# Optimization experiments

Measured on AMD Instinct MI355X. Metric: run time of the kernel, lower is better.

Reference implementation:

```python
import jax, jax.numpy as jnp
import numpy as np

B, S, H, NH = 2, 2048, 1024, 16
HD = H // NH  # 64
BASE = 10000.0


def _rope_tables(seq_len, head_dim):
    inv_freq = 1.0 / (BASE ** (jnp.arange(0, head_dim, 2, dtype=jnp.float32) / head_dim))
    t = jnp.arange(seq_len, dtype=jnp.float32)
    freqs = jnp.outer(t, inv_freq)            # [S, HD/2]
    emb = jnp.concatenate([freqs, freqs], -1)  # [S, HD]
    return jnp.cos(emb), jnp.sin(emb)


def _rotate_half(x):
    x1, x2 = jnp.split(x, 2, axis=-1)
    return jnp.concatenate([-x2, x1], axis=-1)


def setup_inputs() -> dict:
    key = jax.random.key(0)
    ks = jax.random.split(key, 5)
    sc = 1.0 / np.sqrt(H)
    return {
        "hidden_states": jax.random.normal(ks[0], (B, S, H), jnp.float32),
        "Wq": jax.random.normal(ks[1], (H, H), jnp.float32) * sc,
        "Wk": jax.random.normal(ks[2], (H, H), jnp.float32) * sc,
        "Wv": jax.random.normal(ks[3], (H, H), jnp.float32) * sc,
        "Wo": jax.random.normal(ks[4], (H, H), jnp.float32) * sc,
    }


def reference(hidden_states, Wq, Wk, Wv, Wo):
    b, s, h = hidden_states.shape
    # nn.Linear: y = x @ W.T
    q = hidden_states @ Wq.T
    k = hidden_states @ Wk.T
    v = hidden_states @ Wv.T
    # [B, NH, S, HD]
    q = q.reshape(b, s, NH, HD).transpose(0, 2, 1, 3)
    k = k.reshape(b, s, NH, HD).transpose(0, 2, 1, 3)
    v = v.reshape(b, s, NH, HD).transpose(0, 2, 1, 3)
    cos, sin = _rope_tables(s, HD)  # [S, HD], broadcast over B, NH
    q = q * cos + _rotate_half(q) * sin
    k = k * cos + _rotate_half(k) * sin
    scores = jnp.einsum('bhqd,bhkd->bhqk', q, k) / jnp.sqrt(jnp.float32(HD))
    probs = jax.nn.softmax(scores, axis=-1)
    ctx = jnp.einsum('bhqk,bhkd->bhqd', probs, v)
    ctx = ctx.transpose(0, 2, 1, 3).reshape(b, s, h)
    return ctx @ Wo.T
```

## Files before the change

### kernel.cpp

```cpp
#include <hip/hip_runtime.h>
#include <hip/hip_bf16.h>
#include <math.h>

typedef __hip_bfloat16 bf16;
typedef float f32x4 __attribute__((ext_vector_type(4)));
typedef float f32x16 __attribute__((ext_vector_type(16)));
typedef short s16x8 __attribute__((ext_vector_type(8)));

#define NB 2
#define SEQ 2048
#define HID 1024
#define NHEAD 16
#define HD 64
#define BH (NB * NHEAD)
#define MROWS (NB * SEQ)
#define QSCL 0.18033688011111793f

static __device__ __forceinline__ f32x4 mfma16(s16x8 a, s16x8 b, f32x4 c) {
  return __builtin_amdgcn_mfma_f32_16x16x32_bf16(a, b, c, 0, 0, 0);
}
static __device__ __forceinline__ f32x16 mfma32(s16x8 a, s16x8 b, f32x16 c) {
  return __builtin_amdgcn_mfma_f32_32x32x16_bf16(a, b, c, 0, 0, 0);
}

static __device__ __forceinline__ void gload_lds16(const bf16* g, bf16* l) {
  __builtin_amdgcn_global_load_lds((const __attribute__((address_space(1))) void*)g,
                                   (__attribute__((address_space(3))) void*)l, 16, 0, 0);
}

static __device__ __forceinline__ unsigned pack_bf16(float a, float b) {
  __hip_bfloat162 t = __float22bfloat162_rn(float2{a, b});
  return *(unsigned*)&t;
}

__global__ __launch_bounds__(256) void prep_kernel(const float* __restrict__ X,
                                                   const float* __restrict__ wq, const float* __restrict__ wk,
                                                   const float* __restrict__ wv, const float* __restrict__ wo,
                                                   bf16* __restrict__ Xb, bf16* __restrict__ wqkv,
                                                   bf16* __restrict__ wob,
                                                   float* __restrict__ ct, float* __restrict__ st) {
  int bid = blockIdx.x, tid = threadIdx.x;
  if (bid < 8192) {
    const float* src;
    bf16* dst;
    int i;
    if (bid < 4096) {
      src = X; dst = Xb;
      i = (bid * 256 + tid) * 4;
    } else {
      int wsel = (bid - 4096) >> 10;
      src = (wsel == 0) ? wq : (wsel == 1) ? wk : (wsel == 2) ? wv : wo;
      dst = (wsel < 3) ? (wqkv + (size_t)wsel * HID * HID) : wob;
      i = (((bid - 4096) & 1023) * 256 + tid) * 4;
    }
    float4 v = *(const float4*)(src + i);
    bf16 a0 = __float2bfloat16(v.x), a1 = __float2bfloat16(v.y);
    bf16 a2 = __float2bfloat16(v.z), a3 = __float2bfloat16(v.w);
    ushort4 u;
    u.x = *(const unsigned short*)&a0;
    u.y = *(const unsigned short*)&a1;
    u.z = *(const unsigned short*)&a2;
    u.w = *(const unsigned short*)&a3;
    *(ushort4*)(dst + i) = u;
  } else {
    int i = (bid - 8192) * 256 + tid;
    int s = i >> 5, j = i & 31;
    float inv = expf(-(float)(2 * j) * (9.210340371976184f / 64.0f));
    float ang = (float)s * inv;
    float sn, cs;
    sincosf(ang, &sn, &cs);
    ct[i] = cs;
    st[i] = sn;
  }
}

template <int MODE>
__global__ __launch_bounds__(256) void gemm_bt(const bf16* __restrict__ A, const bf16* __restrict__ Bm,
                                               float* __restrict__ C,
                                               bf16* __restrict__ Qb, bf16* __restrict__ Kb,
                                               bf16* __restrict__ Vtg,
                                               const float* __restrict__ ct, const float* __restrict__ st,
                                               int M, int N, int K) {
  __shared__ __align__(16) bf16 As[128][32];
  __shared__ __align__(16) bf16 Bs[128][32];
  const int tid = threadIdx.x, lane = tid & 63, wid = tid >> 6;
  const int wm = wid >> 1, wn = wid & 1;
  const int tm = blockIdx.y * 128, tn = blockIdx.x * 128;
  const int lrow = lane >> 2;
  const int lcol = (lane & 3) * 8;

  f32x4 acc[4][4];
#pragma unroll
  for (int i = 0; i < 4; ++i)
#pragma unroll
    for (int j = 0; j < 4; ++j) acc[i][j] = (f32x4){0.f, 0.f, 0.f, 0.f};

  for (int k0 = 0; k0 < K; k0 += 32) {
    __syncthreads();
    {
      int r0 = wid * 32;
      gload_lds16(A  + (size_t)(tm + r0 +      lrow) * K + k0 + lcol, &As[r0][0]);
      gload_lds16(A  + (size_t)(tm + r0 + 16 + lrow) * K + k0 + lcol, &As[r0 + 16][0]);
      gload_lds16(Bm + (size_t)(tn + r0 +      lrow) * K + k0 + lcol, &Bs[r0][0]);
      gload_lds16(Bm + (size_t)(tn + r0 + 16 + lrow) * K + k0 + lcol, &Bs[r0 + 16][0]);
    }
    __syncthreads();
    s16x8 af[4], bfr[4];
#pragma unroll
    for (int mi = 0; mi < 4; ++mi)
      af[mi] = *(const s16x8*)&As[wm * 64 + mi * 16 + (lane & 15)][(lane >> 4) * 8];
#pragma unroll
    for (int ni = 0; ni < 4; ++ni)
      bfr[ni] = *(const s16x8*)&Bs[wn * 64 + ni * 16 + (lane & 15)][(lane >> 4) * 8];
#pragma unroll
    for (int mi = 0; mi < 4; ++mi)
#pragma unroll
      for (int ni = 0; ni < 4; ++ni)
        acc[mi][ni] = mfma16(af[mi], bfr[ni], acc[mi][ni]);
  }

  if (MODE == 0) {
    const int tblk = tn >> 10;
    if (tblk < 2) {
      const float scl = (tblk == 0) ? QSCL : 1.0f;
#pragma unroll
      for (int mi = 0; mi < 4; ++mi) {
#pragma unroll
        for (int r = 0; r < 4; ++r) {
          int row = tm + wm * 64 + mi * 16 + (lane >> 4) * 4 + r;
          int s = row & (SEQ - 1);
#pragma unroll
          for (int p = 0; p < 2; ++p) {
            int j = p * 16 + (lane & 15);
            float c = ct[s * 32 + j], sn = st[s * 32 + j];
            float x0 = acc[mi][p][r], x1 = acc[mi][p + 2][r];
            acc[mi][p][r]     = (x0 * c - x1 * sn) * scl;
            acc[mi][p + 2][r] = (x1 * c + x0 * sn) * scl;
          }
        }
      }
    }
  }

#pragma unroll
  for (int mi = 0; mi < 4; ++mi) {
#pragma unroll
    for (int ni = 0; ni < 4; ++ni) {
#pragma unroll
      for (int r = 0; r < 4; ++r) {
        int row = tm + wm * 64 + mi * 16 + (lane >> 4) * 4 + r;
        int col = tn + wn * 64 + ni * 16 + (lane & 15);
        float v = acc[mi][ni][r];
        if (MODE == 0) {
          int t = col >> 10, c = col & (HID - 1);
          int h = c >> 6, d = c & 63;
          int b = row >> 11, s = row & (SEQ - 1);
          size_t bh = (size_t)(b * NHEAD + h);
          if (t == 0)      Qb[(bh * SEQ + s) * HD + d]  = __float2bfloat16(v);
          else if (t == 1) Kb[(bh * SEQ + s) * HD + d]  = __float2bfloat16(v);
          else             Vtg[(bh * HD + d) * SEQ + s] = __float2bfloat16(v);
        } else {
          C[(size_t)row * N + col] = v;
        }
      }
    }
  }
}

__global__ __launch_bounds__(512, 2) void attn_kernel(const bf16* __restrict__ Q, const bf16* __restrict__ K,
                                                      const bf16* __restrict__ Vt, bf16* __restrict__ ctx) {
  __shared__ __align__(16) bf16 S[65536];
  const int tid = threadIdx.x, l = tid & 63, w = tid >> 6;
  const int lq = l & 31, hi = l >> 5;
  const int grp = w >> 2, wq = w & 3;
  const int gtid = tid & 255;

  const int id = blockIdx.x;
  const int lin = (id & 7) * 64 + (id >> 3);
  const int bh = lin >> 4, qb = lin & 15;

  const bf16* Qp  = Q  + ((size_t)bh * SEQ + qb * 128) * HD;
  const bf16* Kp0 = K  + (size_t)bh * SEQ * HD;
  const bf16* Vp0 = Vt + (size_t)bh * HD * SEQ;

  bf16* Ksg = S + grp * 32768;
  bf16* Vsg = S + grp * 32768 + 16384;

  s16x8 qf[4];
  {
    const bf16* qr = Qp + (wq * 32 + lq) * HD + hi * 8;
#pragma unroll
    for (int ks = 0; ks < 4; ++ks) qf[ks] = *(const s16x8*)(qr + ks * 16);
  }

  const int s0 = gtid, s1 = gtid + 256;
  const int R0 = s0 >> 3, R1 = s1 >> 3;
  const int c0 = ((s0 & 7) ^ (R0 & 7)) * 8;
  const int c1 = ((s1 & 7) ^ (R1 & 7)) * 8;
  const int p0 = (R0 & 51) | ((R0 & 4) << 1) | ((R0 & 8) >> 1);
  const int p1 = (R1 & 51) | ((R1 & 4) << 1) | ((R1 & 8) >> 1);
  const bf16* kS0 = Kp0 + p0 * HD + c0;
  const bf16* kS1 = Kp0 + p1 * HD + c1;
  const bf16* vS0 = Vp0 + (size_t)R0 * SEQ + c0;
  const bf16* vS1 = Vp0 + (size_t)R1 * SEQ + c1;

#define STAGE(t, b)                                                        \
  do {                                                                     \
    gload_lds16(kS0 + (size_t)(t) * (64 * HD), Ksg + (b) * 4096 + s0 * 8); \
    gload_lds16(kS1 + (size_t)(t) * (64 * HD), Ksg + (b) * 4096 + s1 * 8); \
    gload_lds16(vS0 + (t) * 64,                Vsg + (b) * 4096 + s0 * 8); \
    gload_lds16(vS1 + (t) * 64,                Vsg + (b) * 4096 + s1 * 8); \
  } while (0)

  const int base = grp * 16;
  STAGE(base + 0, 0);
  STAGE(base + 1, 1);

  float m_run = -INFINITY, lsum = 0.f;
  f32x16 acc0{}, acc1{};

#define PROCESS(sf0, sf1, pf)                                                        \
  do {                                                                               \
    float mx[16];                                                                    \
    _Pragma("unroll") for (int i = 0; i < 16; ++i) mx[i] = fmaxf(sf0[i], sf1[i]);    \
    _Pragma("unroll") for (int w2 = 8; w2 >= 1; w2 >>= 1)                            \
      _Pragma("unroll") for (int i = 0; i < 8; ++i)                                  \
        if (i < w2) mx[i] = fmaxf(mx[i], mx[i + w2]);                                \
    float pmax = fmaxf(mx[0], __shfl_xor(mx[0], 32));                                \
    if (__any(pmax > m_run + 8.f)) {                                                 \
      float mn = fmaxf(m_run, pmax);                                                 \
      float corr = __builtin_amdgcn_exp2f(m_run - mn);                               \
      m_run = mn;                                                                    \
      lsum *= corr;                                                                  \
      _Pragma("unroll") for (int r = 0; r < 16; ++r) {                               \
        float cr = __shfl(corr, (r & 3) + 8 * (r >> 2) + 4 * hi);                    \
        acc0[r] *= cr;                                                               \
        acc1[r] *= cr;                                                               \
      }                                                                              \
    }                                                                                \
    _Pragma("unroll") for (int i = 0; i < 16; ++i) sf0[i] = __builtin_amdgcn_exp2f(sf0[i] - m_run); \
    _Pragma("unroll") for (int i = 0; i < 16; ++i) sf1[i] = __builtin_amdgcn_exp2f(sf1[i] - m_run); \
    float sm[16];                                                                    \
    _Pragma("unroll") for (int i = 0; i < 16; ++i) sm[i] = sf0[i] + sf1[i];          \
    _Pragma("unroll") for (int w2 = 8; w2 >= 1; w2 >>= 1)                            \
      _Pragma("unroll") for (int i = 0; i < 8; ++i)                                  \
        if (i < w2) sm[i] += sm[i + w2];                                             \
    lsum += sm[0];                                                                   \
    _Pragma("unroll") for (int kt = 0; kt < 4; ++kt) {                               \
      union { unsigned u[4]; s16x8 v; } cc;                                          \
      _Pragma("unroll") for (int vv = 0; vv < 4; ++vv) {                             \
        if (kt < 2) cc.u[vv] = pack_bf16(sf0[(kt & 1) * 8 + 2 * vv], sf0[(kt & 1) * 8 + 2 * vv + 1]); \
        else        cc.u[vv] = pack_bf16(sf1[(kt & 1) * 8 + 2 * vv], sf1[(kt & 1) * 8 + 2 * vv + 1]); \
      }                                                                              \
      pf[kt] = cc.v;                                                                 \
    }                                                                                \
  } while (0)

  for (int ss = 0; ss < 8; ++ss) {
    const int bufA = (ss & 1) * 2, bufB = bufA + 1;
    __builtin_amdgcn_s_barrier();
    if (ss < 7) {
      STAGE(base + 2 * ss + 2, (bufA + 2) & 3);
      STAGE(base + 2 * ss + 3, (bufB + 2) & 3);
      asm volatile("s_waitcnt vmcnt(8)" ::: "memory");
    } else {
      asm volatile("s_waitcnt vmcnt(0)" ::: "memory");
    }
    __builtin_amdgcn_sched_barrier(0);
    __builtin_amdgcn_s_barrier();

    const bf16* KcA = Ksg + bufA * 4096;
    const bf16* VcA = Vsg + bufA * 4096;
    const bf16* KcB = Ksg + bufB * 4096;
    const bf16* VcB = Vsg + bufB * 4096;

    f32x16 sA0{}, sA1{}, sB0{}, sB1{};
    __builtin_amdgcn_s_setprio(1);
#pragma unroll
    for (int ks = 0; ks < 4; ++ks) {
      const int slot = (ks * 2 + hi) ^ (lq & 7);
      sA0 = mfma32(*(const s16x8*)(KcA + lq * 64 + slot * 8),        qf[ks], sA0);
      sA1 = mfma32(*(const s16x8*)(KcA + (32 + lq) * 64 + slot * 8), qf[ks], sA1);
    }
#pragma unroll
    for (int ks = 0; ks < 4; ++ks) {
      const int slot = (ks * 2 + hi) ^ (lq & 7);
      sB0 = mfma32(*(const s16x8*)(KcB + lq * 64 + slot * 8),        qf[ks], sB0);
      sB1 = mfma32(*(const s16x8*)(KcB + (32 + lq) * 64 + slot * 8), qf[ks], sB1);
    }
    __builtin_amdgcn_s_setprio(0);

    s16x8 pfA[4];
    PROCESS(sA0, sA1, pfA);
    __builtin_amdgcn_s_setprio(1);
#pragma unroll
    for (int kt = 0; kt < 4; ++kt) {
      const int slot = (kt * 2 + hi) ^ (lq & 7);
      acc0 = mfma32(pfA[kt], *(const s16x8*)(VcA + lq * 64 + slot * 8),        acc0);
      acc1 = mfma32(pfA[kt], *(const s16x8*)(VcA + (32 + lq) * 64 + slot * 8), acc1);
    }
    __builtin_amdgcn_s_setprio(0);

    s16x8 pfB[4];
    PROCESS(sB0, sB1, pfB);
    __builtin_amdgcn_s_setprio(1);
#pragma unroll
    for (int kt = 0; kt < 4; ++kt) {
      const int slot = (kt * 2 + hi) ^ (lq & 7);
      acc0 = mfma32(pfB[kt], *(const s16x8*)(VcB + lq * 64 + slot * 8),        acc0);
      acc1 = mfma32(pfB[kt], *(const s16x8*)(VcB + (32 + lq) * 64 + slot * 8), acc1);
    }
    __builtin_amdgcn_s_setprio(0);
  }
#undef STAGE
#undef PROCESS

  lsum += __shfl_xor(lsum, 32);

  __syncthreads();

  float* Op = (float*)(S + 32768);
  float* Mp = (float*)(S);
  float* Lp = Mp + 128;

  if (grp == 1) {
    if (hi == 0) {
      Mp[wq * 32 + lq] = m_run;
      Lp[wq * 32 + lq] = lsum;
    }
#pragma unroll
    for (int r = 0; r < 16; ++r) {
      int q = (r & 3) + 8 * (r >> 2) + 4 * hi;
      Op[(wq * 32 + q) * 64 + lq]      = acc0[r];
      Op[(wq * 32 + q) * 64 + 32 + lq] = acc1[r];
    }
  }
  __syncthreads();

  if (grp == 0) {
    float m1 = Mp[wq * 32 + lq], l1 = Lp[wq * 32 + lq];
    float mN = fmaxf(m_run, m1);
    float cr0 = __builtin_amdgcn_exp2f(m_run - mN);
    float cr1 = __builtin_amdgcn_exp2f(m1 - mN);
    float inv = 1.0f / (lsum * cr0 + l1 * cr1);

    const int b = bh >> 4, h = bh & (NHEAD - 1);
#pragma unroll
    for (int r = 0; r < 16; ++r) {
      int q = (r & 3) + 8 * (r >> 2) + 4 * hi;
      float c0q = __shfl(cr0, q);
      float c1q = __shfl(cr1, q);
      float invq = __shfl(inv, q);
      float o0 = (acc0[r] * c0q + Op[(wq * 32 + q) * 64 + lq]      * c1q) * invq;
      float o1 = (acc1[r] * c0q + Op[(wq * 32 + q) * 64 + 32 + lq] * c1q) * invq;
      size_t base2 = ((size_t)b * SEQ + qb * 128 + wq * 32 + q) * HID + h * HD + lq;
      ctx[base2]      = __float2bfloat16(o0);
      ctx[base2 + 32] = __float2bfloat16(o1);
    }
  }
}

extern "C" void kernel_launch(void* const* d_in, const int* in_sizes, int n_in,
                              void* d_out, int out_size, void* d_ws, size_t ws_size,
                              hipStream_t stream) {
  const float* X  = (const float*)d_in[0];
  const float* Wq = (const float*)d_in[1];
  const float* Wk = (const float*)d_in[2];
  const float* Wv = (const float*)d_in[3];
  const float* Wo = (const float*)d_in[4];

  char* p = (char*)d_ws;
  bf16* Xb   = (bf16*)p; p += (size_t)MROWS * HID * 2;
  bf16* Wqkv = (bf16*)p; p += (size_t)3 * HID * HID * 2;
  bf16* Wob  = (bf16*)p; p += (size_t)HID * HID * 2;
  bf16* Qb   = (bf16*)p; p += (size_t)BH * SEQ * HD * 2;
  bf16* Kb   = (bf16*)p; p += (size_t)BH * SEQ * HD * 2;
  bf16* Vtg  = (bf16*)p; p += (size_t)BH * HD * SEQ * 2;
  bf16* Cb   = (bf16*)p; p += (size_t)MROWS * HID * 2;
  float* ct  = (float*)p; p += (size_t)SEQ * 32 * 4;
  float* st  = (float*)p; p += (size_t)SEQ * 32 * 4;

  prep_kernel<<<8448, 256, 0, stream>>>(X, Wq, Wk, Wv, Wo, Xb, Wqkv, Wob, ct, st);

  gemm_bt<0><<<dim3(3 * HID / 128, MROWS / 128), 256, 0, stream>>>(
      Xb, Wqkv, nullptr, Qb, Kb, Vtg, ct, st, MROWS, 3 * HID, HID);

  attn_kernel<<<dim3(512), 512, 0, stream>>>(Qb, Kb, Vtg, Cb);

  gemm_bt<1><<<dim3(HID / 128, MROWS / 128), 256, 0, stream>>>(
      Cb, Wob, (float*)d_out, nullptr, nullptr, nullptr, nullptr, nullptr, MROWS, HID, HID);
}
```

Measured before the change: 145.6 us.

## Process two query tiles per attention block to reuse staged K/V tiles

Result: slower. 552.6 us (+279.4%).

```diff
diff --git a/kernel.cpp b/kernel.cpp
--- a/kernel.cpp
+++ b/kernel.cpp
@@ -167,30 +167,34 @@
   }
 }
 
-__global__ __launch_bounds__(512, 2) void attn_kernel(const bf16* __restrict__ Q, const bf16* __restrict__ K,
+__global__ __launch_bounds__(512, 4) void attn_kernel(const bf16* __restrict__ Q, const bf16* __restrict__ K,
                                                       const bf16* __restrict__ Vt, bf16* __restrict__ ctx) {
-  __shared__ __align__(16) bf16 S[65536];
+  __shared__ __align__(16) bf16 S[32768];
   const int tid = threadIdx.x, l = tid & 63, w = tid >> 6;
   const int lq = l & 31, hi = l >> 5;
   const int grp = w >> 2, wq = w & 3;
   const int gtid = tid & 255;
 
   const int id = blockIdx.x;
-  const int lin = (id & 7) * 64 + (id >> 3);
-  const int bh = lin >> 4, qb = lin & 15;
-
-  const bf16* Qp  = Q  + ((size_t)bh * SEQ + qb * 128) * HD;
+  const int lin = (id & 7) * 32 + (id >> 3);
+  const int bh = lin >> 3, qb = lin & 7;
+
+  const bf16* Qp  = Q  + ((size_t)bh * SEQ + qb * 256) * HD;
   const bf16* Kp0 = K  + (size_t)bh * SEQ * HD;
   const bf16* Vp0 = Vt + (size_t)bh * HD * SEQ;
 
-  bf16* Ksg = S + grp * 32768;
-  bf16* Vsg = S + grp * 32768 + 16384;
-
-  s16x8 qf[4];
+  bf16* Ksg = S + grp * 16384;
+  bf16* Vsg = S + grp * 16384 + 8192;
+
+  s16x8 qf0[4], qf1[4];
   {
-    const bf16* qr = Qp + (wq * 32 + lq) * HD + hi * 8;
-#pragma unroll
-    for (int ks = 0; ks < 4; ++ks) qf[ks] = *(const s16x8*)(qr + ks * 16);
+    const bf16* qr0 = Qp + (wq * 32 + lq) * HD + hi * 8;
+    const bf16* qr1 = Qp + (128 + wq * 32 + lq) * HD + hi * 8;
+#pragma unroll
+    for (int ks = 0; ks < 4; ++ks) {
+      qf0[ks] = *(const s16x8*)(qr0 + ks * 16);
+      qf1[ks] = *(const s16x8*)(qr1 + ks * 16);
+    }
   }
 
   const int s0 = gtid, s1 = gtid + 256;
@@ -212,14 +216,7 @@
     gload_lds16(vS1 + (t) * 64,                Vsg + (b) * 4096 + s1 * 8); \
   } while (0)
 
-  const int base = grp * 16;
-  STAGE(base + 0, 0);
-  STAGE(base + 1, 1);
-
-  float m_run = -INFINITY, lsum = 0.f;
-  f32x16 acc0{}, acc1{};
-
-#define PROCESS(sf0, sf1, pf)                                                        \
+#define PROCESS(sf0, sf1, pf, m_run, lsum, acc0, acc1)                               \
   do {                                                                               \
     float mx[16];                                                                    \
     _Pragma("unroll") for (int i = 0; i < 16; ++i) mx[i] = fmaxf(sf0[i], sf1[i]);    \
@@ -256,108 +253,127 @@
     }                                                                                \
   } while (0)
 
-  for (int ss = 0; ss < 8; ++ss) {
-    const int bufA = (ss & 1) * 2, bufB = bufA + 1;
+  const int base = grp * 16;
+  STAGE(base + 0, 0);
+
+  float m0 = -INFINITY, l0 = 0.f, m1 = -INFINITY, l1 = 0.f;
+  f32x16 a00{}, a01{}, a10{}, a11{};
+
+  const int NSTEP = 16;
+  for (int t = 0; t < NSTEP; ++t) {
+    const int cur = t & 1;
     __builtin_amdgcn_s_barrier();
-    if (ss < 7) {
-      STAGE(base + 2 * ss + 2, (bufA + 2) & 3);
-      STAGE(base + 2 * ss + 3, (bufB + 2) & 3);
-      asm volatile("s_waitcnt vmcnt(8)" ::: "memory");
+    if (t + 1 < NSTEP) {
+      STAGE(base + t + 1, cur ^ 1);
+      asm volatile("s_waitcnt vmcnt(4)" ::: "memory");
     } else {
       asm volatile("s_waitcnt vmcnt(0)" ::: "memory");
     }
     __builtin_amdgcn_sched_barrier(0);
     __builtin_amdgcn_s_barrier();
 
-    const bf16* KcA = Ksg + bufA * 4096;
-    const bf16* VcA = Vsg + bufA * 4096;
-    const bf16* KcB = Ksg + bufB * 4096;
-    const bf16* VcB = Vsg + bufB * 4096;
-
-    f32x16 sA0{}, sA1{}, sB0{}, sB1{};
-    __builtin_amdgcn_s_setprio(1);
+    const bf16* Kc = Ksg + cur * 4096;
+    const bf16* Vc = Vsg + cur * 4096;
+
+    s16x8 kf[8], vf[8];
 #pragma unroll
     for (int ks = 0; ks < 4; ++ks) {
       const int slot = (ks * 2 + hi) ^ (lq & 7);
-      sA0 = mfma32(*(const s16x8*)(KcA + lq * 64 + slot * 8),        qf[ks], sA0);
-      sA1 = mfma32(*(const s16x8*)(KcA + (32 + lq) * 64 + slot * 8), qf[ks], sA1);
-    }
-#pragma unroll
-    for (int ks = 0; ks < 4; ++ks) {
-      const int slot = (ks * 2 + hi) ^ (lq & 7);
-      sB0 = mfma32(*(const s16x8*)(KcB + lq * 64 + slot * 8),        qf[ks], sB0);
-      sB1 = mfma32(*(const s16x8*)(KcB + (32 + lq) * 64 + slot * 8), qf[ks], sB1);
-    }
-    __builtin_amdgcn_s_setprio(0);
-
-    s16x8 pfA[4];
-    PROCESS(sA0, sA1, pfA);
-    __builtin_amdgcn_s_setprio(1);
-#pragma unroll
-    for (int kt = 0; kt < 4; ++kt) {
-      const int slot = (kt * 2 + hi) ^ (lq & 7);
-      acc0 = mfma32(pfA[kt], *(const s16x8*)(VcA + lq * 64 + slot * 8),        acc0);
-      acc1 = mfma32(pfA[kt], *(const s16x8*)(VcA + (32 + lq) * 64 + slot * 8), acc1);
-    }
-    __builtin_amdgcn_s_setprio(0);
-
-    s16x8 pfB[4];
-    PROCESS(sB0, sB1, pfB);
-    __builtin_amdgcn_s_setprio(1);
-#pragma unroll
-    for (int kt = 0; kt < 4; ++kt) {
-      const int slot = (kt * 2 + hi) ^ (lq & 7);
-      acc0 = mfma32(pfB[kt], *(const s16x8*)(VcB + lq * 64 + slot * 8),        acc0);
-      acc1 = mfma32(pfB[kt], *(const s16x8*)(VcB + (32 + lq) * 64 + slot * 8), acc1);
-    }
-    __builtin_amdgcn_s_setprio(0);
+      kf[ks * 2]     = *(const s16x8*)(Kc + lq * 64 + slot * 8);
+      kf[ks * 2 + 1] = *(const s16x8*)(Kc + (32 + lq) * 64 + slot * 8);
+      vf[ks * 2]     = *(const s16x8*)(Vc + lq * 64 + slot * 8);
+      vf[ks * 2 + 1] = *(const s16x8*)(Vc + (32 + lq) * 64 + slot * 8);
+    }
+
+    {
+      f32x16 sf0{}, sf1{};
+      __builtin_amdgcn_s_setprio(1);
+#pragma unroll
+      for (int ks = 0; ks < 4; ++ks) {
+        sf0 = mfma32(kf[ks * 2],     qf0[ks], sf0);
+        sf1 = mfma32(kf[ks * 2 + 1], qf0[ks], sf1);
+      }
+      __builtin_amdgcn_s_setprio(0);
+      s16x8 pf[4];
+      PROCESS(sf0, sf1, pf, m0, l0, a00, a01);
+      __builtin_amdgcn_s_setprio(1);
+#pragma unroll
+      for (int kt = 0; kt < 4; ++kt) {
+        a00 = mfma32(pf[kt], vf[kt * 2],     a00);
+        a01 = mfma32(pf[kt], vf[kt * 2 + 1], a01);
+      }
+      __builtin_amdgcn_s_setprio(0);
+    }
+
+    {
+      f32x16 sf0{}, sf1{};
+      __builtin_amdgcn_s_setprio(1);
+#pragma unroll
+      for (int ks = 0; ks < 4; ++ks) {
+        sf0 = mfma32(kf[ks * 2],     qf1[ks], sf0);
+        sf1 = mfma32(kf[ks * 2 + 1], qf1[ks], sf1);
+      }
+      __builtin_amdgcn_s_setprio(0);
+      s16x8 pf[4];
+      PROCESS(sf0, sf1, pf, m1, l1, a10, a11);
+      __builtin_amdgcn_s_setprio(1);
+#pragma unroll
+      for (int kt = 0; kt < 4; ++kt) {
+        a10 = mfma32(pf[kt], vf[kt * 2],     a10);
+        a11 = mfma32(pf[kt], vf[kt * 2 + 1], a11);
+      }
+      __builtin_amdgcn_s_setprio(0);
+    }
   }
 #undef STAGE
 #undef PROCESS
 
-  lsum += __shfl_xor(lsum, 32);
-
-  __syncthreads();
-
-  float* Op = (float*)(S + 32768);
-  float* Mp = (float*)(S);
+  l0 += __shfl_xor(l0, 32);
+  l1 += __shfl_xor(l1, 32);
+
+  float* Op = (float*)(S + 16384);
+  float* Mp = (float*)S;
   float* Lp = Mp + 128;
-
-  if (grp == 1) {
-    if (hi == 0) {
-      Mp[wq * 32 + lq] = m_run;
-      Lp[wq * 32 + lq] = lsum;
-    }
-#pragma unroll
-    for (int r = 0; r < 16; ++r) {
-      int q = (r & 3) + 8 * (r >> 2) + 4 * hi;
-      Op[(wq * 32 + q) * 64 + lq]      = acc0[r];
-      Op[(wq * 32 + q) * 64 + 32 + lq] = acc1[r];
-    }
-  }
-  __syncthreads();
-
-  if (grp == 0) {
-    float m1 = Mp[wq * 32 + lq], l1 = Lp[wq * 32 + lq];
-    float mN = fmaxf(m_run, m1);
-    float cr0 = __builtin_amdgcn_exp2f(m_run - mN);
-    float cr1 = __builtin_amdgcn_exp2f(m1 - mN);
-    float inv = 1.0f / (lsum * cr0 + l1 * cr1);
-
-    const int b = bh >> 4, h = bh & (NHEAD - 1);
-#pragma unroll
-    for (int r = 0; r < 16; ++r) {
-      int q = (r & 3) + 8 * (r >> 2) + 4 * hi;
-      float c0q = __shfl(cr0, q);
-      float c1q = __shfl(cr1, q);
-      float invq = __shfl(inv, q);
-      float o0 = (acc0[r] * c0q + Op[(wq * 32 + q) * 64 + lq]      * c1q) * invq;
-      float o1 = (acc1[r] * c0q + Op[(wq * 32 + q) * 64 + 32 + lq] * c1q) * invq;
-      size_t base2 = ((size_t)b * SEQ + qb * 128 + wq * 32 + q) * HID + h * HD + lq;
-      ctx[base2]      = __float2bfloat16(o0);
-      ctx[base2 + 32] = __float2bfloat16(o1);
-    }
-  }
+  const int b = bh >> 4, h = bh & (NHEAD - 1);
+
+#define MERGE_PHASE(m_run, lsum, acc0, acc1, QOFF)                                   \
+  do {                                                                               \
+    __syncthreads();                                                                 \
+    if (grp == 1) {                                                                  \
+      if (hi == 0) {                                                                 \
+        Mp[wq * 32 + lq] = m_run;                                                    \
+        Lp[wq * 32 + lq] = lsum;                                                     \
+      }                                                                              \
+      _Pragma("unroll") for (int r = 0; r < 16; ++r) {                               \
+        int q = (r & 3) + 8 * (r >> 2) + 4 * hi;                                     \
+        Op[(wq * 32 + q) * 64 + lq]      = acc0[r];                                  \
+        Op[(wq * 32 + q) * 64 + 32 + lq] = acc1[r];                                  \
+      }                                                                              \
+    }                                                                                \
+    __syncthreads();                                                                 \
+    if (grp == 0) {                                                                  \
+      float m1x = Mp[wq * 32 + lq], l1x = Lp[wq * 32 + lq];                          \
+      float mN = fmaxf(m_run, m1x);                                                  \
+      float cr0 = __builtin_amdgcn_exp2f(m_run - mN);                                \
+      float cr1 = __builtin_amdgcn_exp2f(m1x - mN);                                  \
+      float inv = 1.0f / (lsum * cr0 + l1x * cr1);                                   \
+      _Pragma("unroll") for (int r = 0; r < 16; ++r) {                               \
+        int q = (r & 3) + 8 * (r >> 2) + 4 * hi;                                     \
+        float c0q = __shfl(cr0, q);                                                  \
+        float c1q = __shfl(cr1, q);                                                  \
+        float invq = __shfl(inv, q);                                                 \
+        float o0 = (acc0[r] * c0q + Op[(wq * 32 + q) * 64 + lq]      * c1q) * invq;  \
+        float o1 = (acc1[r] * c0q + Op[(wq * 32 + q) * 64 + 32 + lq] * c1q) * invq;  \
+        size_t base2 = ((size_t)b * SEQ + qb * 256 + (QOFF) + wq * 32 + q) * HID + h * HD + lq; \
+        ctx[base2]      = __float2bfloat16(o0);                                      \
+        ctx[base2 + 32] = __float2bfloat16(o1);                                      \
+      }                                                                              \
+    }                                                                                \
+  } while (0)
+
+  MERGE_PHASE(m0, l0, a00, a01, 0);
+  MERGE_PHASE(m1, l1, a10, a11, 128);
+#undef MERGE_PHASE
 }
 
 extern "C" void kernel_launch(void* const* d_in, const int* in_sizes, int n_in,
@@ -385,7 +401,7 @@
   gemm_bt<0><<<dim3(3 * HID / 128, MROWS / 128), 256, 0, stream>>>(
       Xb, Wqkv, nullptr, Qb, Kb, Vtg, ct, st, MROWS, 3 * HID, HID);
 
-  attn_kernel<<<dim3(512), 512, 0, stream>>>(Qb, Kb, Vtg, Cb);
+  attn_kernel<<<dim3(256), 512, 0, stream>>>(Qb, Kb, Vtg, Cb);
 
   gemm_bt<1><<<dim3(HID / 128, MROWS / 128), 256, 0, stream>>>(
       Cb, Wob, (float*)d_out, nullptr, nullptr, nullptr, nullptr, nullptr, MROWS, HID, HID);
```

## Software-pipeline attention loop with half LDS and higher occupancy

Applied to the files above, without the earlier changes.

Measured after the change: 159.1 us. 9.3% more time.

```diff
diff --git a/kernel.cpp b/kernel.cpp
--- a/kernel.cpp
+++ b/kernel.cpp
@@ -31,6 +31,10 @@
 static __device__ __forceinline__ unsigned pack_bf16(float a, float b) {
   __hip_bfloat162 t = __float22bfloat162_rn(float2{a, b});
   return *(unsigned*)&t;
+}
+
+static __device__ __forceinline__ float max3f(float a, float b, float c) {
+  return fmaxf(fmaxf(a, b), c);
 }
 
 __global__ __launch_bounds__(256) void prep_kernel(const float* __restrict__ X,
@@ -167,9 +171,9 @@
   }
 }
 
-__global__ __launch_bounds__(512, 2) void attn_kernel(const bf16* __restrict__ Q, const bf16* __restrict__ K,
+__global__ __launch_bounds__(512, 4) void attn_kernel(const bf16* __restrict__ Q, const bf16* __restrict__ K,
                                                       const bf16* __restrict__ Vt, bf16* __restrict__ ctx) {
-  __shared__ __align__(16) bf16 S[65536];
+  __shared__ __align__(16) bf16 S[32768];
   const int tid = threadIdx.x, l = tid & 63, w = tid >> 6;
   const int lq = l & 31, hi = l >> 5;
   const int grp = w >> 2, wq = w & 3;
@@ -183,8 +187,8 @@
   const bf16* Kp0 = K  + (size_t)bh * SEQ * HD;
   const bf16* Vp0 = Vt + (size_t)bh * HD * SEQ;
 
-  bf16* Ksg = S + grp * 32768;
-  bf16* Vsg = S + grp * 32768 + 16384;
+  bf16* Ksg = S + grp * 16384;
+  bf16* Vsg = S + grp * 16384 + 8192;
 
   s16x8 qf[4];
   {
@@ -195,8 +199,8 @@
 
   const int s0 = gtid, s1 = gtid + 256;
   const int R0 = s0 >> 3, R1 = s1 >> 3;
-  const int c0 = ((s0 & 7) ^ (R0 & 7)) * 8;
-  const int c1 = ((s1 & 7) ^ (R1 & 7)) * 8;
+  const int c0 = (((s0 & 7) ^ (R0 & 7) ^ ((R0 >> 3) & 3))) * 8;
+  const int c1 = (((s1 & 7) ^ (R1 & 7) ^ ((R1 >> 3) & 3))) * 8;
   const int p0 = (R0 & 51) | ((R0 & 4) << 1) | ((R0 & 8) >> 1);
   const int p1 = (R1 & 51) | ((R1 & 4) << 1) | ((R1 & 8) >> 1);
   const bf16* kS0 = Kp0 + p0 * HD + c0;
@@ -212,21 +216,19 @@
     gload_lds16(vS1 + (t) * 64,                Vsg + (b) * 4096 + s1 * 8); \
   } while (0)
 
-  const int base = grp * 16;
-  STAGE(base + 0, 0);
-  STAGE(base + 1, 1);
-
-  float m_run = -INFINITY, lsum = 0.f;
-  f32x16 acc0{}, acc1{};
-
 #define PROCESS(sf0, sf1, pf)                                                        \
   do {                                                                               \
-    float mx[16];                                                                    \
-    _Pragma("unroll") for (int i = 0; i < 16; ++i) mx[i] = fmaxf(sf0[i], sf1[i]);    \
-    _Pragma("unroll") for (int w2 = 8; w2 >= 1; w2 >>= 1)                            \
-      _Pragma("unroll") for (int i = 0; i < 8; ++i)                                  \
-        if (i < w2) mx[i] = fmaxf(mx[i], mx[i + w2]);                                \
-    float pmax = fmaxf(mx[0], __shfl_xor(mx[0], 32));                                \
+    float v0[16];                                                                    \
+    _Pragma("unroll") for (int i = 0; i < 16; ++i) v0[i] = fmaxf(sf0[i], sf1[i]);    \
+    float t0 = max3f(v0[0], v0[1], v0[2]);                                           \
+    float t1 = max3f(v0[3], v0[4], v0[5]);                                           \
+    float t2 = max3f(v0[6], v0[7], v0[8]);                                           \
+    float t3 = max3f(v0[9], v0[10], v0[11]);                                         \
+    float t4 = max3f(v0[12], v0[13], v0[14]);                                        \
+    float u0 = max3f(t0, t1, v0[15]);                                                \
+    float u1 = max3f(t2, t3, t4);                                                    \
+    float um = fmaxf(u0, u1);                                                        \
+    float pmax = fmaxf(um, __shfl_xor(um, 32));                                      \
     if (__any(pmax > m_run + 8.f)) {                                                 \
       float mn = fmaxf(m_run, pmax);                                                 \
       float corr = __builtin_amdgcn_exp2f(m_run - mn);                               \
@@ -256,70 +258,78 @@
     }                                                                                \
   } while (0)
 
-  for (int ss = 0; ss < 8; ++ss) {
-    const int bufA = (ss & 1) * 2, bufB = bufA + 1;
+  const int base = grp * 16;
+  STAGE(base + 0, 0);
+
+  float m_run = -INFINITY, lsum = 0.f;
+  f32x16 acc0{}, acc1{};
+  f32x16 sf0{}, sf1{};
+  s16x8 vf[8];
+
+  const int rsx = (lq & 7) ^ ((lq >> 3) & 3);
+
+  const int NSTEP = 16;
+  for (int t = 0; t < NSTEP; ++t) {
+    const int cur = t & 1;
     __builtin_amdgcn_s_barrier();
-    if (ss < 7) {
-      STAGE(base + 2 * ss + 2, (bufA + 2) & 3);
-      STAGE(base + 2 * ss + 3, (bufB + 2) & 3);
-      asm volatile("s_waitcnt vmcnt(8)" ::: "memory");
+    if (t + 1 < NSTEP) {
+      STAGE(base + t + 1, cur ^ 1);
+      asm volatile("s_waitcnt vmcnt(4)" ::: "memory");
     } else {
       asm volatile("s_waitcnt vmcnt(0)" ::: "memory");
     }
     __builtin_amdgcn_sched_barrier(0);
     __builtin_amdgcn_s_barrier();
 
-    const bf16* KcA = Ksg + bufA * 4096;
-    const bf16* VcA = Vsg + bufA * 4096;
-    const bf16* KcB = Ksg + bufB * 4096;
-    const bf16* VcB = Vsg + bufB * 4096;
-
-    f32x16 sA0{}, sA1{}, sB0{}, sB1{};
+    const bf16* Kc = Ksg + cur * 4096;
+    const bf16* Vc = Vsg + cur * 4096;
+
+    s16x8 pf[4];
+    if (t > 0) PROCESS(sf0, sf1, pf);
+
+    sf0 = (f32x16){};
+    sf1 = (f32x16){};
     __builtin_amdgcn_s_setprio(1);
 #pragma unroll
     for (int ks = 0; ks < 4; ++ks) {
-      const int slot = (ks * 2 + hi) ^ (lq & 7);
-      sA0 = mfma32(*(const s16x8*)(KcA + lq * 64 + slot * 8),        qf[ks], sA0);
-      sA1 = mfma32(*(const s16x8*)(KcA + (32 + lq) * 64 + slot * 8), qf[ks], sA1);
-    }
-#pragma unroll
-    for (int ks = 0; ks < 4; ++ks) {
-      const int slot = (ks * 2 + hi) ^ (lq & 7);
-      sB0 = mfma32(*(const s16x8*)(KcB + lq * 64 + slot * 8),        qf[ks], sB0);
-      sB1 = mfma32(*(const s16x8*)(KcB + (32 + lq) * 64 + slot * 8), qf[ks], sB1);
+      const int slot = (ks * 2 + hi) ^ rsx;
+      sf0 = mfma32(*(const s16x8*)(Kc + lq * 64 + slot * 8),        qf[ks], sf0);
+      sf1 = mfma32(*(const s16x8*)(Kc + (32 + lq) * 64 + slot * 8), qf[ks], sf1);
+    }
+    if (t > 0) {
+#pragma unroll
+      for (int kt = 0; kt < 4; ++kt) {
+        acc0 = mfma32(pf[kt], vf[kt * 2],     acc0);
+        acc1 = mfma32(pf[kt], vf[kt * 2 + 1], acc1);
+      }
     }
     __builtin_amdgcn_s_setprio(0);
 
-    s16x8 pfA[4];
-    PROCESS(sA0, sA1, pfA);
-    __builtin_amdgcn_s_setprio(1);
 #pragma unroll
     for (int kt = 0; kt < 4; ++kt) {
-      const int slot = (kt * 2 + hi) ^ (lq & 7);
-      acc0 = mfma32(pfA[kt], *(const s16x8*)(VcA + lq * 64 + slot * 8),        acc0);
-      acc1 = mfma32(pfA[kt], *(const s16x8*)(VcA + (32 + lq) * 64 + slot * 8), acc1);
-    }
-    __builtin_amdgcn_s_setprio(0);
-
-    s16x8 pfB[4];
-    PROCESS(sB0, sB1, pfB);
-    __builtin_amdgcn_s_setprio(1);
+      const int slot = (kt * 2 + hi) ^ rsx;
+      vf[kt * 2]     = *(const s16x8*)(Vc + lq * 64 + slot * 8);
+      vf[kt * 2 + 1] = *(const s16x8*)(Vc + (32 + lq) * 64 + slot * 8);
+    }
+  }
+#undef STAGE
+
+  {
+    s16x8 pf[4];
+    PROCESS(sf0, sf1, pf);
 #pragma unroll
     for (int kt = 0; kt < 4; ++kt) {
-      const int slot = (kt * 2 + hi) ^ (lq & 7);
-      acc0 = mfma32(pfB[kt], *(const s16x8*)(VcB + lq * 64 + slot * 8),        acc0);
-      acc1 = mfma32(pfB[kt], *(const s16x8*)(VcB + (32 + lq) * 64 + slot * 8), acc1);
-    }
-    __builtin_amdgcn_s_setprio(0);
-  }
-#undef STAGE
+      acc0 = mfma32(pf[kt], vf[kt * 2],     acc0);
+      acc1 = mfma32(pf[kt], vf[kt * 2 + 1], acc1);
+    }
+  }
 #undef PROCESS
 
   lsum += __shfl_xor(lsum, 32);
 
   __syncthreads();
 
-  float* Op = (float*)(S + 32768);
+  float* Op = (float*)(S + 16384);
   float* Mp = (float*)(S);
   float* Lp = Mp + 128;
 
```
